# Optimization experiments

Measured on AMD Instinct MI355X. Metric: run time of the kernel, lower is better.

The kernel has to match this reference:

```python
import jax, jax.numpy as jnp
import numpy as np

B, N, V, H, Z = 2048, 32, 10, 256, 64


def setup_inputs() -> dict:
    key = jax.random.key(0)
    ks = jax.random.split(key, 14)
    # strictly upper-triangular random DAG adjacency (topological order = vertex index)
    p = jax.random.uniform(ks[0], (B, N, N))
    tri = jnp.triu(jnp.ones((N, N), jnp.float32), k=1)
    adj = (p < 0.12).astype(jnp.float32) * tri
    node_types = jax.random.randint(ks[1], (B, N), 0, V).astype(jnp.int32)
    s = 0.05
    return dict(
        adj=adj,
        node_types=node_types,
        w_ih=jax.random.normal(ks[2], (V, 3 * H), jnp.float32) * s,
        w_hh=jax.random.normal(ks[3], (H, 3 * H), jnp.float32) * s,
        b_ih=jax.random.normal(ks[4], (3 * H,), jnp.float32) * s,
        b_hh=jax.random.normal(ks[5], (3 * H,), jnp.float32) * s,
        w_gate=jax.random.normal(ks[6], (H, H), jnp.float32) * s,
        b_gate=jax.random.normal(ks[7], (H,), jnp.float32) * s,
        w_map=jax.random.normal(ks[8], (H, H), jnp.float32) * s,
        w_mu=jax.random.normal(ks[9], (H, Z), jnp.float32) * s,
        b_mu=jax.random.normal(ks[10], (Z,), jnp.float32) * s,
        w_std=jax.random.normal(ks[11], (H, Z), jnp.float32) * s,
        b_std=jax.random.normal(ks[12], (Z,), jnp.float32) * s,
    )


def _gru_cell(x, h, w_ih, w_hh, b_ih, b_hh):
    # torch GRUCell math; weights stored [in, 3H]
    gi = x @ w_ih + b_ih  # [B, 3H]
    gh = h @ w_hh + b_hh
    i_r, i_z, i_n = jnp.split(gi, 3, axis=-1)
    h_r, h_z, h_n = jnp.split(gh, 3, axis=-1)
    r = jax.nn.sigmoid(i_r + h_r)
    z = jax.nn.sigmoid(i_z + h_z)
    n = jnp.tanh(i_n + r * h_n)
    return (1.0 - z) * n + z * h


def reference(adj, node_types, w_ih, w_hh, b_ih, b_hh, w_gate, b_gate, w_map,
              w_mu, b_mu, w_std, b_std):
    x_all = jax.nn.one_hot(node_types, V, dtype=adj.dtype)  # [B, N, V]
    hidden0 = jnp.zeros((B, N, H), adj.dtype)
    adj_cols = jnp.transpose(adj, (2, 0, 1))  # [N, B, N]; col v = predecessor mask of v
    x_seq = jnp.transpose(x_all, (1, 0, 2))   # [N, B, V]

    def step(hidden, inps):
        col, x, v = inps
        # gate(h_pred) * map(h_pred), summed over predecessors. map has no bias,
        # so non-predecessor (zero-masked) rows contribute exactly zero, matching
        # the padded-gather formulation in the original code.
        gm = jax.nn.sigmoid(hidden @ w_gate + b_gate) * (hidden @ w_map)  # [B, N, H]
        agg = jnp.einsum('bn,bnh->bh', col, gm)  # [B, H]; zero for v=0 (no preds)
        h_new = _gru_cell(x, agg, w_ih, w_hh, b_ih, b_hh)  # [B, H]
        hidden = jax.lax.dynamic_update_slice(hidden, h_new[:, None, :], (0, v, 0))
        return hidden, None

    hidden, _ = jax.lax.scan(step, hidden0, (adj_cols, x_seq, jnp.arange(N)))
    hg = hidden[:, -1, :]  # graph state = last vertex hidden
    mu = hg @ w_mu + b_mu
    sigma = hg @ w_std + b_std
    return (mu, sigma)
```

## Files before the change

### kernel.cpp

```cpp
#include <hip/hip_runtime.h>


#define BB 2048
#define NN 32
#define VV 10
#define HH 256
#define ZZ 64
#define BT 8
#define KC 8
#define NT1 48
#define NT2 32
#define WHH_ELEMS (NT1 * KC * 64 * 8)
#define WGM_ELEMS (NT2 * KC * 64 * 8)

typedef __attribute__((ext_vector_type(8))) short frag8;
typedef __attribute__((ext_vector_type(4))) float facc4;
typedef __attribute__((ext_vector_type(4))) unsigned short us4;
typedef __attribute__((ext_vector_type(4))) unsigned int ui4;

__device__ __forceinline__ float bf2f(unsigned short u) {
    unsigned int x = ((unsigned int)u) << 16;
    return __builtin_bit_cast(float, x);
}
__device__ __forceinline__ unsigned short f2bf(float f) {
    unsigned int x = __builtin_bit_cast(unsigned int, f);
    x += 0x7FFFu + ((x >> 16) & 1u);
    return (unsigned short)(x >> 16);
}
__device__ __forceinline__ float sigm(float x) { return 1.0f / (1.0f + __expf(-x)); }
__device__ __forceinline__ float ldv(const float* p, size_t i) { return p[i]; }
__device__ __forceinline__ float ldv(const unsigned short* p, size_t i) { return bf2f(p[i]); }
__device__ __forceinline__ void stv(float* p, size_t i, float v) { p[i] = v; }
__device__ __forceinline__ void stv(unsigned short* p, size_t i, float v) { p[i] = f2bf(v); }

__device__ __forceinline__ void pin_frag(frag8& f) {
    ui4 t = __builtin_bit_cast(ui4, f);
    asm volatile("" : "+v"(t));
    f = __builtin_bit_cast(frag8, t);
}

__global__ void detect_dtype(const unsigned short* __restrict__ w, int* flag) {
    __shared__ int zc, bc;
    if (threadIdx.x == 0) { zc = 0; bc = 0; }
    __syncthreads();
    int z = 0, b = 0;
    for (int i = threadIdx.x; i < 2048; i += 256) {
        unsigned short lo = w[2 * i];
        if (lo == 0) z++;
        unsigned e = (lo >> 7) & 0xFFu;
        if (e >= 0x86u) b++;
    }
    atomicAdd(&zc, z); atomicAdd(&bc, b);
    __syncthreads();
    if (threadIdx.x == 0) *flag = (bc > 0 || zc > 512) ? 1 : 0;
}

template <typename T>
__global__ void repack_weights(const T* __restrict__ w_hh,
                               const T* __restrict__ w_gate,
                               const T* __restrict__ w_map,
                               const T* __restrict__ w_ih,
                               const T* __restrict__ b_ih,
                               unsigned short* __restrict__ whh_p,
                               unsigned short* __restrict__ wgm_p,
                               float* __restrict__ wihG,
                               const int* __restrict__ flag, int want) {
    if (*flag != want) return;
    int t = blockIdx.x * blockDim.x + threadIdx.x;
    int lane = t & 63;
    int frag = t >> 6;
    int kbase = (lane >> 4) * 8;
    if (frag < NT1 * KC) {
        int jt = frag / KC, kc = frag % KC;
        int col = jt * 16 + (lane & 15);
        unsigned short* dst = whh_p + ((size_t)frag * 64 + lane) * 8;
        #pragma unroll
        for (int j = 0; j < 8; ++j)
            dst[j] = f2bf(ldv(w_hh, (size_t)(kc * 32 + kbase + j) * 768 + col));
    } else if (frag < (NT1 + NT2) * KC) {
        int f2 = frag - NT1 * KC;
        int jt = f2 / KC, kc = f2 % KC;
        int col = jt * 16 + (lane & 15);
        unsigned short* dst = wgm_p + ((size_t)f2 * 64 + lane) * 8;
        #pragma unroll
        for (int j = 0; j < 8; ++j) {
            int k = kc * 32 + kbase + j;
            dst[j] = f2bf((col < HH) ? ldv(w_gate, (size_t)k * HH + col)
                                     : ldv(w_map, (size_t)k * HH + (col - HH)));
        }
    } else {
        int idx = t - (NT1 + NT2) * KC * 64;
        if (idx < VV * 768) {
            int c = idx % 768;
            wihG[idx] = ldv(w_ih, (size_t)idx) + ldv(b_ih, (size_t)c);
        }
    }
}

template <typename T>
__global__ __launch_bounds__(512)
__attribute__((amdgpu_waves_per_eu(2, 2)))
void vae_main(
    const T* __restrict__ adj,
    const int* __restrict__ ntypes,
    const T* __restrict__ b_hh,
    const T* __restrict__ b_gate,
    const T* __restrict__ w_mu,
    const T* __restrict__ b_mu,
    const T* __restrict__ w_std,
    const T* __restrict__ b_std,
    const unsigned short* __restrict__ whh_p,
    const unsigned short* __restrict__ wgm_p,
    const float* __restrict__ wihG,
    T* __restrict__ out,
    const int* __restrict__ flag, int want)
{
    if (*flag != want) return;

    __shared__ __align__(16) unsigned short gmAll[BT][NN][HH];
    __shared__ __align__(16) unsigned short aggbf[16][264];
    __shared__ __align__(16) unsigned short hnew[16][264];
    __shared__ unsigned int  amask[BT][NN];
    __shared__ int           ntva[BT][NN];
    __shared__ __align__(16) float bhhL[768];
    __shared__ float bgL[HH];

    float* const aggA = (float*)&aggbf[8][0];
    float* const aggB = (float*)&hnew[8][0];

    const int tid  = threadIdx.x;
    const int lane = tid & 63;
    const int w    = tid >> 6;
    const int b0   = blockIdx.x * BT;

    const frag8* whh8 = (const frag8*)whh_p;
    const frag8* wgm8 = (const frag8*)wgm_p;

    if (tid < 256) {
        int bi = tid >> 5, vv = tid & 31;
        unsigned m = 0;
        for (int n = 0; n < NN; ++n)
            if (ldv(adj, ((size_t)(b0 + bi) * NN + n) * NN + vv) != 0.0f) m |= (1u << n);
        amask[bi][vv] = m;
    } else {
        int idx = tid - 256;
        int bi = idx >> 5, vv = idx & 31;
        ntva[bi][vv] = ntypes[(b0 + bi) * NN + vv];
    }
    for (int i = tid; i < 768; i += 512) bhhL[i] = ldv(b_hh, i);
    if (tid < HH) bgL[tid] = ldv(b_gate, tid);

    frag8 wHH[6][KC];
    #pragma unroll
    for (int s = 0; s < 2; ++s)
        #pragma unroll
        for (int g = 0; g < 3; ++g) {
            const frag8* p = whh8 + (size_t)(w + 8 * s + 16 * g) * (KC * 64) + lane;
            #pragma unroll
            for (int kc = 0; kc < KC; ++kc) wHH[s * 3 + g][kc] = p[kc * 64];
        }
    #pragma unroll
    for (int i = 0; i < 6; ++i)
        #pragma unroll
        for (int kc = 0; kc < KC; ++kc) pin_frag(wHH[i][kc]);
    __syncthreads();

    for (int v = 0; v < NN; ++v) {
        {
            const int bi = w;
            const int h4 = lane * 4;
            unsigned m = amask[bi][v];
            float a0 = 0.f, a1 = 0.f, a2 = 0.f, a3 = 0.f;
            const unsigned short* rb = &gmAll[bi][0][0] + h4;
            while (m) {
                const int n0 = __builtin_ctz(m); m &= m - 1;
                const us4 g0 = *(const us4*)(rb + n0 * HH);
                if (m) {
                    const int n1 = __builtin_ctz(m); m &= m - 1;
                    const us4 g1 = *(const us4*)(rb + n1 * HH);
                    a0 += bf2f(g0.x) + bf2f(g1.x);
                    a1 += bf2f(g0.y) + bf2f(g1.y);
                    a2 += bf2f(g0.z) + bf2f(g1.z);
                    a3 += bf2f(g0.w) + bf2f(g1.w);
                } else {
                    a0 += bf2f(g0.x); a1 += bf2f(g0.y);
                    a2 += bf2f(g0.z); a3 += bf2f(g0.w);
                }
            }
            float* ap = (bi < 4) ? (aggA + bi * 256) : (aggB + (bi - 4) * 256);
            *(float4*)(ap + h4) = make_float4(a0, a1, a2, a3);
            ushort4 ab; ab.x = f2bf(a0); ab.y = f2bf(a1); ab.z = f2bf(a2); ab.w = f2bf(a3);
            *(ushort4*)&aggbf[bi][h4] = ab;
        }
        __syncthreads();

        #pragma unroll
        for (int s = 0; s < 2; ++s) {
            const int t = w + 8 * s;
            const int col = t * 16 + (lane & 15);
            const int q = lane >> 4;

            facc4 aR = {0.f, 0.f, 0.f, 0.f};
            facc4 aZ = {0.f, 0.f, 0.f, 0.f};
            facc4 aN = {0.f, 0.f, 0.f, 0.f};
            #pragma unroll
            for (int kc = 0; kc < KC; ++kc) {
                const frag8 af = *(const frag8*)&aggbf[lane & 15][kc * 32 + (lane >> 4) * 8];
                aR = __builtin_amdgcn_mfma_f32_16x16x32_bf16(af, wHH[s * 3 + 0][kc], aR, 0, 0, 0);
                aZ = __builtin_amdgcn_mfma_f32_16x16x32_bf16(af, wHH[s * 3 + 1][kc], aZ, 0, 0, 0);
                aN = __builtin_amdgcn_mfma_f32_16x16x32_bf16(af, wHH[s * 3 + 2][kc], aN, 0, 0, 0);
            }
            if (q < 2) {
                const float bhr = bhhL[col], bhz = bhhL[col + 256], bhn = bhhL[col + 512];
                const float* ap = (q == 0) ? aggA : aggB;
                #pragma unroll
                for (int i = 0; i < 4; ++i) {
                    const float* wr = wihG + (size_t)ntva[4 * q + i][v] * 768 + col;
                    const float r = sigm(wr[0]   + aR[i] + bhr);
                    const float z = sigm(wr[256] + aZ[i] + bhz);
                    const float n = tanhf(wr[512] + r * (aN[i] + bhn));
                    hnew[4 * q + i][col] = f2bf((1.f - z) * n + z * ap[i * 256 + col]);
                }
            }
        }
        __syncthreads();

        {
            facc4 aG0 = {0.f, 0.f, 0.f, 0.f};
            facc4 aG1 = {0.f, 0.f, 0.f, 0.f};
            facc4 aM0 = {0.f, 0.f, 0.f, 0.f};
            facc4 aM1 = {0.f, 0.f, 0.f, 0.f};
            const frag8* pG0 = wgm8 + (size_t)(w     ) * (KC * 64) + lane;
            const frag8* pG1 = wgm8 + (size_t)(w +  8) * (KC * 64) + lane;
            const frag8* pM0 = wgm8 + (size_t)(w + 16) * (KC * 64) + lane;
            const frag8* pM1 = wgm8 + (size_t)(w + 24) * (KC * 64) + lane;
            #pragma unroll
            for (int kc = 0; kc < KC; ++kc) {
                const frag8 hf = *(const frag8*)&hnew[lane & 15][kc * 32 + (lane >> 4) * 8];
                aG0 = __builtin_amdgcn_mfma_f32_16x16x32_bf16(hf, pG0[kc * 64], aG0, 0, 0, 0);
                aG1 = __builtin_amdgcn_mfma_f32_16x16x32_bf16(hf, pG1[kc * 64], aG1, 0, 0, 0);
                aM0 = __builtin_amdgcn_mfma_f32_16x16x32_bf16(hf, pM0[kc * 64], aM0, 0, 0, 0);
                aM1 = __builtin_amdgcn_mfma_f32_16x16x32_bf16(hf, pM1[kc * 64], aM1, 0, 0, 0);
            }
            const int q = lane >> 4;
            if (q < 2) {
                const int c0 = w * 16 + (lane & 15);
                const int c1 = (w + 8) * 16 + (lane & 15);
                const float bg0 = bgL[c0], bg1 = bgL[c1];
                #pragma unroll
                for (int i = 0; i < 4; ++i) {
                    gmAll[4 * q + i][v][c0] = f2bf(sigm(aG0[i] + bg0) * aM0[i]);
                    gmAll[4 * q + i][v][c1] = f2bf(sigm(aG1[i] + bg1) * aM1[i]);
                }
            }
        }
        __syncthreads();
    }

    {
        const int bi = w, z = lane;
        float am = 0.f, as = 0.f;
        #pragma unroll 4
        for (int h = 0; h < HH; ++h) {
            const float hv = bf2f(hnew[bi][h]);
            am += hv * ldv(w_mu, (size_t)h * ZZ + z);
            as += hv * ldv(w_std, (size_t)h * ZZ + z);
        }
        stv(out, (size_t)(b0 + bi) * ZZ + z, am + ldv(b_mu, z));
        stv(out, (size_t)BB * ZZ + (size_t)(b0 + bi) * ZZ + z, as + ldv(b_std, z));
    }
}

extern "C" void kernel_launch(void* const* d_in, const int* in_sizes, int n_in,
                              void* d_out, int out_size, void* d_ws, size_t ws_size,
                              hipStream_t stream)
{
    unsigned short* whh_p = (unsigned short*)d_ws;
    unsigned short* wgm_p = whh_p + WHH_ELEMS;
    float* wihG = (float*)(wgm_p + WGM_ELEMS);

    size_t flag_off = (ws_size >= 8) ? ((ws_size - 4) & ~(size_t)3) : 0;
    int* flag = (int*)((char*)d_ws + flag_off);

    detect_dtype<<<dim3(1), 256, 0, stream>>>((const unsigned short*)d_in[2], flag);

    repack_weights<float><<<dim3(190), 256, 0, stream>>>(
        (const float*)d_in[3], (const float*)d_in[6], (const float*)d_in[8],
        (const float*)d_in[2], (const float*)d_in[4],
        whh_p, wgm_p, wihG, flag, 1);
    repack_weights<unsigned short><<<dim3(190), 256, 0, stream>>>(
        (const unsigned short*)d_in[3], (const unsigned short*)d_in[6],
        (const unsigned short*)d_in[8], (const unsigned short*)d_in[2],
        (const unsigned short*)d_in[4],
        whh_p, wgm_p, wihG, flag, 0);

    vae_main<float><<<dim3(BB / BT), 512, 0, stream>>>(
        (const float*)d_in[0], (const int*)d_in[1],
        (const float*)d_in[5], (const float*)d_in[7],
        (const float*)d_in[9], (const float*)d_in[10],
        (const float*)d_in[11], (const float*)d_in[12],
        whh_p, wgm_p, wihG, (float*)d_out, flag, 1);
    vae_main<unsigned short><<<dim3(BB / BT), 512, 0, stream>>>(
        (const unsigned short*)d_in[0], (const int*)d_in[1],
        (const unsigned short*)d_in[5], (const unsigned short*)d_in[7],
        (const unsigned short*)d_in[9], (const unsigned short*)d_in[10],
        (const unsigned short*)d_in[11], (const unsigned short*)d_in[12],
        whh_p, wgm_p, wihG, (unsigned short*)d_out, flag, 0);
}
```

Baseline: 601.8 us.

## Stream W_hh from global and overlap predecessor aggregation with gate matmul

Stops pinning the W_hh MFMA fragments in registers for the whole kernel and drops the waves_per_eu(2,2) attribute, reloading W_hh fragments from global/L2 on every step instead. The predecessor aggregation for step v+1 (all predecessors except v) now runs in the same phase as the gate/map MFMAs of step v. The contribution of vertex v is added at the start of the next step, which takes the long LDS gather off the critical sync chain. A and H fragments are also preloaded from LDS into register arrays. The trade is extra global/L2 traffic for W_hh on each step and a changed register/occupancy balance.

```diff
diff --git a/kernel.cpp b/kernel.cpp
--- a/kernel.cpp
+++ b/kernel.cpp
@@ -16,7 +16,6 @@
 typedef __attribute__((ext_vector_type(8))) short frag8;
 typedef __attribute__((ext_vector_type(4))) float facc4;
 typedef __attribute__((ext_vector_type(4))) unsigned short us4;
-typedef __attribute__((ext_vector_type(4))) unsigned int ui4;
 
 __device__ __forceinline__ float bf2f(unsigned short u) {
     unsigned int x = ((unsigned int)u) << 16;
@@ -32,12 +31,6 @@
 __device__ __forceinline__ float ldv(const unsigned short* p, size_t i) { return bf2f(p[i]); }
 __device__ __forceinline__ void stv(float* p, size_t i, float v) { p[i] = v; }
 __device__ __forceinline__ void stv(unsigned short* p, size_t i, float v) { p[i] = f2bf(v); }
-
-__device__ __forceinline__ void pin_frag(frag8& f) {
-    ui4 t = __builtin_bit_cast(ui4, f);
-    asm volatile("" : "+v"(t));
-    f = __builtin_bit_cast(frag8, t);
-}
 
 __global__ void detect_dtype(const unsigned short* __restrict__ w, int* flag) {
     __shared__ int zc, bc;
@@ -98,9 +91,7 @@
 }
 
 template <typename T>
-__global__ __launch_bounds__(512)
-__attribute__((amdgpu_waves_per_eu(2, 2)))
-void vae_main(
+__global__ __launch_bounds__(512) void vae_main(
     const T* __restrict__ adj,
     const int* __restrict__ ntypes,
     const T* __restrict__ b_hh,
@@ -149,83 +140,94 @@
     }
     for (int i = tid; i < 768; i += 512) bhhL[i] = ldv(b_hh, i);
     if (tid < HH) bgL[tid] = ldv(b_gate, tid);
-
-    frag8 wHH[6][KC];
-    #pragma unroll
-    for (int s = 0; s < 2; ++s)
-        #pragma unroll
-        for (int g = 0; g < 3; ++g) {
-            const frag8* p = whh8 + (size_t)(w + 8 * s + 16 * g) * (KC * 64) + lane;
-            #pragma unroll
-            for (int kc = 0; kc < KC; ++kc) wHH[s * 3 + g][kc] = p[kc * 64];
-        }
-    #pragma unroll
-    for (int i = 0; i < 6; ++i)
-        #pragma unroll
-        for (int kc = 0; kc < KC; ++kc) pin_frag(wHH[i][kc]);
     __syncthreads();
+
+    float pa0 = 0.f, pa1 = 0.f, pa2 = 0.f, pa3 = 0.f;
+    const int h4 = lane * 4;
 
     for (int v = 0; v < NN; ++v) {
         {
             const int bi = w;
-            const int h4 = lane * 4;
-            unsigned m = amask[bi][v];
-            float a0 = 0.f, a1 = 0.f, a2 = 0.f, a3 = 0.f;
-            const unsigned short* rb = &gmAll[bi][0][0] + h4;
-            while (m) {
-                const int n0 = __builtin_ctz(m); m &= m - 1;
-                const us4 g0 = *(const us4*)(rb + n0 * HH);
-                if (m) {
-                    const int n1 = __builtin_ctz(m); m &= m - 1;
-                    const us4 g1 = *(const us4*)(rb + n1 * HH);
-                    a0 += bf2f(g0.x) + bf2f(g1.x);
-                    a1 += bf2f(g0.y) + bf2f(g1.y);
-                    a2 += bf2f(g0.z) + bf2f(g1.z);
-                    a3 += bf2f(g0.w) + bf2f(g1.w);
-                } else {
-                    a0 += bf2f(g0.x); a1 += bf2f(g0.y);
-                    a2 += bf2f(g0.z); a3 += bf2f(g0.w);
+            if (v > 0 && ((amask[bi][v] >> (v - 1)) & 1u)) {
+                const us4 g = *(const us4*)(&gmAll[bi][v - 1][0] + h4);
+                pa0 += bf2f(g.x); pa1 += bf2f(g.y);
+                pa2 += bf2f(g.z); pa3 += bf2f(g.w);
+            }
+            float* ap = (bi < 4) ? (aggA + bi * 256) : (aggB + (bi - 4) * 256);
+            *(float4*)(ap + h4) = make_float4(pa0, pa1, pa2, pa3);
+            ushort4 ab; ab.x = f2bf(pa0); ab.y = f2bf(pa1);
+            ab.z = f2bf(pa2); ab.w = f2bf(pa3);
+            *(ushort4*)&aggbf[bi][h4] = ab;
+        }
+        __syncthreads();
+
+        {
+            frag8 afrag[KC];
+            #pragma unroll
+            for (int kc = 0; kc < KC; ++kc)
+                afrag[kc] = *(const frag8*)&aggbf[lane & 15][kc * 32 + (lane >> 4) * 8];
+
+            #pragma unroll
+            for (int s = 0; s < 2; ++s) {
+                const int t = w + 8 * s;
+                const int col = t * 16 + (lane & 15);
+                const int q = lane >> 4;
+
+                facc4 aR = {0.f, 0.f, 0.f, 0.f};
+                facc4 aZ = {0.f, 0.f, 0.f, 0.f};
+                facc4 aN = {0.f, 0.f, 0.f, 0.f};
+                const frag8* pR = whh8 + (size_t)(t     ) * (KC * 64) + lane;
+                const frag8* pZ = whh8 + (size_t)(t + 16) * (KC * 64) + lane;
+                const frag8* pN = whh8 + (size_t)(t + 32) * (KC * 64) + lane;
+                #pragma unroll
+                for (int kc = 0; kc < KC; ++kc) {
+                    aR = __builtin_amdgcn_mfma_f32_16x16x32_bf16(afrag[kc], pR[kc * 64], aR, 0, 0, 0);
+                    aZ = __builtin_amdgcn_mfma_f32_16x16x32_bf16(afrag[kc], pZ[kc * 64], aZ, 0, 0, 0);
+                    aN = __builtin_amdgcn_mfma_f32_16x16x32_bf16(afrag[kc], pN[kc * 64], aN, 0, 0, 0);
                 }
-            }
-            float* ap = (bi < 4) ? (aggA + bi * 256) : (aggB + (bi - 4) * 256);
-            *(float4*)(ap + h4) = make_float4(a0, a1, a2, a3);
-            ushort4 ab; ab.x = f2bf(a0); ab.y = f2bf(a1); ab.z = f2bf(a2); ab.w = f2bf(a3);
-            *(ushort4*)&aggbf[bi][h4] = ab;
+                if (q < 2) {
+                    const float bhr = bhhL[col], bhz = bhhL[col + 256], bhn = bhhL[col + 512];
+                    const float* ap = (q == 0) ? aggA : aggB;
+                    #pragma unroll
+                    for (int i = 0; i < 4; ++i) {
+                        const float* wr = wihG + (size_t)ntva[4 * q + i][v] * 768 + col;
+                        const float r = sigm(wr[0]   + aR[i] + bhr);
+                        const float z = sigm(wr[256] + aZ[i] + bhz);
+                        const float n = tanhf(wr[512] + r * (aN[i] + bhn));
+                        hnew[4 * q + i][col] = f2bf((1.f - z) * n + z * ap[i * 256 + col]);
+                    }
+                }
+            }
         }
         __syncthreads();
 
-        #pragma unroll
-        for (int s = 0; s < 2; ++s) {
-            const int t = w + 8 * s;
-            const int col = t * 16 + (lane & 15);
-            const int q = lane >> 4;
-
-            facc4 aR = {0.f, 0.f, 0.f, 0.f};
-            facc4 aZ = {0.f, 0.f, 0.f, 0.f};
-            facc4 aN = {0.f, 0.f, 0.f, 0.f};
+        {
+            pa0 = pa1 = pa2 = pa3 = 0.f;
+            if (v + 1 < NN) {
+                unsigned m = amask[w][v + 1] & ((1u << v) - 1u);
+                const unsigned short* rb = &gmAll[w][0][0] + h4;
+                while (m) {
+                    const int n0 = __builtin_ctz(m); m &= m - 1;
+                    const us4 g0 = *(const us4*)(rb + n0 * HH);
+                    if (m) {
+                        const int n1 = __builtin_ctz(m); m &= m - 1;
+                        const us4 g1 = *(const us4*)(rb + n1 * HH);
+                        pa0 += bf2f(g0.x) + bf2f(g1.x);
+                        pa1 += bf2f(g0.y) + bf2f(g1.y);
+                        pa2 += bf2f(g0.z) + bf2f(g1.z);
+                        pa3 += bf2f(g0.w) + bf2f(g1.w);
+                    } else {
+                        pa0 += bf2f(g0.x); pa1 += bf2f(g0.y);
+                        pa2 += bf2f(g0.z); pa3 += bf2f(g0.w);
+                    }
+                }
+            }
+
+            frag8 hfrag[KC];
             #pragma unroll
-            for (int kc = 0; kc < KC; ++kc) {
-                const frag8 af = *(const frag8*)&aggbf[lane & 15][kc * 32 + (lane >> 4) * 8];
-                aR = __builtin_amdgcn_mfma_f32_16x16x32_bf16(af, wHH[s * 3 + 0][kc], aR, 0, 0, 0);
-                aZ = __builtin_amdgcn_mfma_f32_16x16x32_bf16(af, wHH[s * 3 + 1][kc], aZ, 0, 0, 0);
-                aN = __builtin_amdgcn_mfma_f32_16x16x32_bf16(af, wHH[s * 3 + 2][kc], aN, 0, 0, 0);
-            }
-            if (q < 2) {
-                const float bhr = bhhL[col], bhz = bhhL[col + 256], bhn = bhhL[col + 512];
-                const float* ap = (q == 0) ? aggA : aggB;
-                #pragma unroll
-                for (int i = 0; i < 4; ++i) {
-                    const float* wr = wihG + (size_t)ntva[4 * q + i][v] * 768 + col;
-                    const float r = sigm(wr[0]   + aR[i] + bhr);
-                    const float z = sigm(wr[256] + aZ[i] + bhz);
-                    const float n = tanhf(wr[512] + r * (aN[i] + bhn));
-                    hnew[4 * q + i][col] = f2bf((1.f - z) * n + z * ap[i * 256 + col]);
-                }
-            }
-        }
-        __syncthreads();
-
-        {
+            for (int kc = 0; kc < KC; ++kc)
+                hfrag[kc] = *(const frag8*)&hnew[lane & 15][kc * 32 + (lane >> 4) * 8];
+
             facc4 aG0 = {0.f, 0.f, 0.f, 0.f};
             facc4 aG1 = {0.f, 0.f, 0.f, 0.f};
             facc4 aM0 = {0.f, 0.f, 0.f, 0.f};
@@ -236,11 +238,10 @@
             const frag8* pM1 = wgm8 + (size_t)(w + 24) * (KC * 64) + lane;
             #pragma unroll
             for (int kc = 0; kc < KC; ++kc) {
-                const frag8 hf = *(const frag8*)&hnew[lane & 15][kc * 32 + (lane >> 4) * 8];
-                aG0 = __builtin_amdgcn_mfma_f32_16x16x32_bf16(hf, pG0[kc * 64], aG0, 0, 0, 0);
-                aG1 = __builtin_amdgcn_mfma_f32_16x16x32_bf16(hf, pG1[kc * 64], aG1, 0, 0, 0);
-                aM0 = __builtin_amdgcn_mfma_f32_16x16x32_bf16(hf, pM0[kc * 64], aM0, 0, 0, 0);
-                aM1 = __builtin_amdgcn_mfma_f32_16x16x32_bf16(hf, pM1[kc * 64], aM1, 0, 0, 0);
+                aG0 = __builtin_amdgcn_mfma_f32_16x16x32_bf16(hfrag[kc], pG0[kc * 64], aG0, 0, 0, 0);
+                aG1 = __builtin_amdgcn_mfma_f32_16x16x32_bf16(hfrag[kc], pG1[kc * 64], aG1, 0, 0, 0);
+                aM0 = __builtin_amdgcn_mfma_f32_16x16x32_bf16(hfrag[kc], pM0[kc * 64], aM0, 0, 0, 0);
+                aM1 = __builtin_amdgcn_mfma_f32_16x16x32_bf16(hfrag[kc], pM1[kc * 64], aM1, 0, 0, 0);
             }
             const int q = lane >> 4;
             if (q < 2) {
```

Result: slower. 644.2 us (+7.0%).
